# Performance work log

Measured on AMD Instinct MI355X. Metric: run time of the kernel, lower is better.

The kernel has to match this reference:

```python
import jax, jax.numpy as jnp
import numpy as np

B, S, D, H = 4, 2048, 1024, 16
DH = D // H  # head dim = 64
MASK_VALUE = -1000000.0


def setup_inputs() -> dict:
    key = jax.random.key(0)
    ks = jax.random.split(key, 8)
    return {
        "key": jax.random.normal(ks[0], (B, S, D), jnp.float32),
        "query": jax.random.normal(ks[1], (B, S, D), jnp.float32),
        "value": jax.random.normal(ks[2], (B, S, D), jnp.float32),
        "valid_lens": jax.random.randint(ks[3], (B,), 0, 2048, jnp.int32),
        # nn.Linear weights stored as [out_features, in_features]
        "Wk": jax.random.normal(ks[4], (D, D), jnp.float32) / np.sqrt(D),
        "Wq": jax.random.normal(ks[5], (D, D), jnp.float32) / np.sqrt(D),
        "Wv": jax.random.normal(ks[6], (D, D), jnp.float32) / np.sqrt(D),
        "Wo": jax.random.normal(ks[7], (D, D), jnp.float32) / np.sqrt(D),
    }


def _split_heads(x):
    # [B, S, D] -> [B, H, S, DH]
    return x.reshape(B, S, H, DH).transpose(0, 2, 1, 3)


def reference(key, query, value, valid_lens, Wk, Wq, Wv, Wo):
    # projections (Linear: x @ W^T, bias=False)
    q = _split_heads(query @ Wq.T)  # [B, H, S, DH]
    k = _split_heads(key @ Wk.T)
    v = _split_heads(value @ Wv.T)

    scale = 1.0 / jnp.sqrt(jnp.asarray(DH, q.dtype))
    scores = jnp.einsum("bhqd,bhkd->bhqk", q, k) * scale  # [B, H, S, S]

    # valid_lens masks the key axis per batch element (same for all heads/queries)
    key_mask = jnp.arange(S) < valid_lens[:, None]  # [B, S]
    scores = jnp.where(key_mask[:, None, None, :], scores, MASK_VALUE)

    attn = jax.nn.softmax(scores, axis=-1)
    out = jnp.einsum("bhqk,bhkd->bhqd", attn, v)  # [B, H, S, DH]
    out = out.transpose(0, 2, 1, 3).reshape(B, S, D)  # concat heads
    return out @ Wo.T
```

## Files before the change

### kernel.cpp

```cpp
#include <hip/hip_runtime.h>
#include <hip/hip_bf16.h>
#include <stdint.h>

typedef __bf16 bf16;
typedef __bf16 bf16x4 __attribute__((ext_vector_type(4)));
typedef __bf16 bf16x8 __attribute__((ext_vector_type(8)));
typedef float f32x4 __attribute__((ext_vector_type(4)));
typedef float f32x8 __attribute__((ext_vector_type(8)));

#define MFMA16 __builtin_amdgcn_mfma_f32_16x16x32_bf16

__device__ __forceinline__ void gload_lds16(void* lds, const void* g) {
  __builtin_amdgcn_global_load_lds(
      (const __attribute__((address_space(1))) unsigned int*)g,
      (__attribute__((address_space(3))) unsigned int*)lds, 16, 0, 0);
}

__global__ __launch_bounds__(256) void cvt1(const float* __restrict__ src,
                                            bf16* __restrict__ dst) {
  int i = (blockIdx.x * 256 + threadIdx.x) * 4;
  f32x4 v = *(const f32x4*)(src + i);
  bf16x4 o;
#pragma unroll
  for (int j = 0; j < 4; j++) o[j] = (bf16)v[j];
  *(bf16x4*)(dst + i) = o;
}

__global__ __launch_bounds__(256) void cvt4(const float* __restrict__ w0,
                                            const float* __restrict__ w1,
                                            const float* __restrict__ w2,
                                            const float* __restrict__ w3,
                                            bf16* __restrict__ dst) {
  const float* srcs[4] = {w0, w1, w2, w3};
  const float* src = srcs[blockIdx.y];
  int i = (blockIdx.x * 256 + threadIdx.x) * 4;
  f32x4 v = *(const f32x4*)(src + i);
  bf16x4 o;
#pragma unroll
  for (int j = 0; j < 4; j++) o[j] = (bf16)v[j];
  *(bf16x4*)(dst + (size_t)blockIdx.y * 1048576 + i) = o;
}

__device__ __forceinline__ void gemm_body(const bf16* __restrict__ A,
                                          const bf16* __restrict__ W,
                                          void* __restrict__ Craw, int mode,
                                          bf16* As, bf16* Bs) {
  constexpr int K = 1024;
  const int t = threadIdx.x;
  const int lane = t & 63;
  const int quad = lane >> 4;
  const int m16 = lane & 15;
  const int w = t >> 6;
  const int m0 = blockIdx.y * 128;
  const int n0 = blockIdx.x * 128;
  const int wm = (w >> 1) * 64;
  const int wn = (w & 1) * 64;

  f32x4 acc[4][4];
#pragma unroll
  for (int i = 0; i < 4; i++)
#pragma unroll
    for (int j = 0; j < 4; j++) acc[i][j] = (f32x4){0.f, 0.f, 0.f, 0.f};

  for (int kt = 0; kt < K / 32; kt++) {
    __syncthreads();
#pragma unroll
    for (int p = 0; p < 2; p++) {
      int idx = p * 256 + t;
      int row = idx >> 2;
      int ce = (idx & 3) * 8;
      gload_lds16(&As[idx * 8], A + (size_t)(m0 + row) * K + kt * 32 + ce);
      gload_lds16(&Bs[idx * 8], W + (size_t)(n0 + row) * K + kt * 32 + ce);
    }
    __syncthreads();

    bf16x8 af[4], bfr[4];
#pragma unroll
    for (int i = 0; i < 4; i++) {
      af[i] = *(const bf16x8*)&As[(wm + i * 16 + m16) * 32 + quad * 8];
      bfr[i] = *(const bf16x8*)&Bs[(wn + i * 16 + m16) * 32 + quad * 8];
    }
#pragma unroll
    for (int i = 0; i < 4; i++)
#pragma unroll
      for (int j = 0; j < 4; j++)
        acc[i][j] = MFMA16(af[i], bfr[j], acc[i][j], 0, 0, 0);
  }

#pragma unroll
  for (int i = 0; i < 4; i++) {
    int rbase = m0 + wm + i * 16 + quad * 4;
#pragma unroll
    for (int j = 0; j < 4; j++) {
      int col = n0 + wn + j * 16 + m16;
#pragma unroll
      for (int r = 0; r < 4; r++) {
        int row = rbase + r;
        if (mode == 0) {
          ((float*)Craw)[(size_t)row * 1024 + col] = acc[i][j][r];
        } else {
          int b = row >> 11, s = row & 2047;
          int h = col >> 6, d = col & 63;
          bf16 v = (bf16)acc[i][j][r];
          if (mode == 1)
            ((bf16*)Craw)[(((size_t)(b * 16 + h)) * 2048 + s) * 64 + d] = v;
          else
            ((bf16*)Craw)[(((size_t)(b * 16 + h)) * 64 + d) * 2048 + s] = v;
        }
      }
    }
  }
}

__global__ __launch_bounds__(256) void gemm_qkv(
    const bf16* __restrict__ xq, const bf16* __restrict__ xk,
    const bf16* __restrict__ xv, const bf16* __restrict__ wb,
    bf16* __restrict__ qp, bf16* __restrict__ kp, bf16* __restrict__ vt) {
  __shared__ bf16 As[128 * 32];
  __shared__ bf16 Bs[128 * 32];
  const int z = blockIdx.z;
  const bf16* A = (z == 0) ? xq : (z == 1) ? xk : xv;
  const bf16* W = wb + (size_t)z * 1048576;
  bf16* C = (z == 0) ? qp : (z == 1) ? kp : vt;
  gemm_body(A, W, C, (z == 2) ? 2 : 1, As, Bs);
}

__global__ __launch_bounds__(256) void gemm_one(const bf16* __restrict__ A,
                                                const bf16* __restrict__ W,
                                                void* __restrict__ Craw,
                                                int mode) {
  __shared__ bf16 As[128 * 32];
  __shared__ bf16 Bs[128 * 32];
  gemm_body(A, W, Craw, mode, As, Bs);
}

template <int AF32, int WF32>
__global__ __launch_bounds__(256) void gemm_bt(const void* __restrict__ Araw,
                                               const void* __restrict__ Wraw,
                                               void* __restrict__ Craw,
                                               int mode) {
  constexpr int K = 1024;
  __shared__ bf16 As[128 * 32];
  __shared__ bf16 Bs[128 * 32];
  const int t = threadIdx.x;
  const int lane = t & 63;
  const int quad = lane >> 4;
  const int m16 = lane & 15;
  const int w = t >> 6;
  const int m0 = blockIdx.y * 128;
  const int n0 = blockIdx.x * 128;
  const int wm = (w >> 1) * 64;
  const int wn = (w & 1) * 64;

  f32x4 acc[4][4];
#pragma unroll
  for (int i = 0; i < 4; i++)
#pragma unroll
    for (int j = 0; j < 4; j++) acc[i][j] = (f32x4){0.f, 0.f, 0.f, 0.f};

  for (int kt = 0; kt < K / 32; kt++) {
    bf16x8 aR[2], bR[2];
#pragma unroll
    for (int p = 0; p < 2; p++) {
      int idx = p * 256 + t;
      int row = idx >> 2;
      int ce = (idx & 3) * 8;
      size_t aoff = (size_t)(m0 + row) * K + kt * 32 + ce;
      size_t boff = (size_t)(n0 + row) * K + kt * 32 + ce;
      if constexpr (AF32) {
        f32x8 av = *(const f32x8*)((const float*)Araw + aoff);
#pragma unroll
        for (int j = 0; j < 8; j++) aR[p][j] = (bf16)av[j];
      } else {
        aR[p] = *(const bf16x8*)((const bf16*)Araw + aoff);
      }
      if constexpr (WF32) {
        f32x8 bv = *(const f32x8*)((const float*)Wraw + boff);
#pragma unroll
        for (int j = 0; j < 8; j++) bR[p][j] = (bf16)bv[j];
      } else {
        bR[p] = *(const bf16x8*)((const bf16*)Wraw + boff);
      }
    }
    __syncthreads();
#pragma unroll
    for (int p = 0; p < 2; p++) {
      int idx = p * 256 + t;
      *(bf16x8*)&As[idx * 8] = aR[p];
      *(bf16x8*)&Bs[idx * 8] = bR[p];
    }
    __syncthreads();

    bf16x8 af[4], bfr[4];
#pragma unroll
    for (int i = 0; i < 4; i++) {
      af[i] = *(const bf16x8*)&As[(wm + i * 16 + m16) * 32 + quad * 8];
      bfr[i] = *(const bf16x8*)&Bs[(wn + i * 16 + m16) * 32 + quad * 8];
    }
#pragma unroll
    for (int i = 0; i < 4; i++)
#pragma unroll
      for (int j = 0; j < 4; j++)
        acc[i][j] = MFMA16(af[i], bfr[j], acc[i][j], 0, 0, 0);
  }

#pragma unroll
  for (int i = 0; i < 4; i++) {
    int rbase = m0 + wm + i * 16 + quad * 4;
#pragma unroll
    for (int j = 0; j < 4; j++) {
      int col = n0 + wn + j * 16 + m16;
#pragma unroll
      for (int r = 0; r < 4; r++) {
        int row = rbase + r;
        if (mode == 0) {
          ((float*)Craw)[(size_t)row * 1024 + col] = acc[i][j][r];
        } else {
          int b = row >> 11, s = row & 2047;
          int h = col >> 6, d = col & 63;
          bf16 v = (bf16)acc[i][j][r];
          if (mode == 1)
            ((bf16*)Craw)[(((size_t)(b * 16 + h)) * 2048 + s) * 64 + d] = v;
          else
            ((bf16*)Craw)[(((size_t)(b * 16 + h)) * 64 + d) * 2048 + s] = v;
        }
      }
    }
  }
}

__global__ __launch_bounds__(256) void attn(const bf16* __restrict__ qp,
                                            const bf16* __restrict__ kp,
                                            const bf16* __restrict__ vt,
                                            const int* __restrict__ vlen,
                                            bf16* __restrict__ ctx) {
  __shared__ bf16 Ks[64 * 64];
  __shared__ bf16 Vs[64 * 64];
  __shared__ bf16 Ps[4 * 16 * 72];

  const int t = threadIdx.x;
  const int lane = t & 63;
  const int quad = lane >> 4;
  const int m16 = lane & 15;
  const int sw = m16 & 7;
  const int w = t >> 6;
  const int bh = blockIdx.y;
  const int qt = blockIdx.x;
  const int b = bh >> 4;
  const int h = bh & 15;
  const int vl = vlen[b];

  const float C1 = 0.18033688f;
  const float C2 = 46.166241f;
  const float mArg = (vl == 0) ? 0.0f : -12800.0f;

  const bf16* qbase = qp + ((size_t)(bh * 2048 + qt * 64 + w * 16 + m16)) * 64;
  bf16x8 qf[2];
  qf[0] = *(const bf16x8*)(qbase + quad * 8);
  qf[1] = *(const bf16x8*)(qbase + 32 + quad * 8);

  float rsum[4] = {0.f, 0.f, 0.f, 0.f};
  f32x4 o[4];
#pragma unroll
  for (int nt = 0; nt < 4; nt++) o[nt] = (f32x4){0.f, 0.f, 0.f, 0.f};

  const int ktEnd = (vl == 0) ? 32 : ((vl + 63) >> 6);

  for (int kt = 0; kt < ktEnd; kt++) {
    __syncthreads();
#pragma unroll
    for (int p = 0; p < 2; p++) {
      int idx = p * 256 + t;
      int row = idx >> 3;
      int gc = (idx & 7) ^ (row & 7);
      gload_lds16(&Ks[idx * 8],
                  &kp[((size_t)(bh * 2048 + kt * 64 + row)) * 64 + gc * 8]);
      gload_lds16(&Vs[idx * 8],
                  &vt[((size_t)(bh * 64 + row)) * 2048 + kt * 64 + gc * 8]);
    }
    __syncthreads();

    f32x4 s[4];
#pragma unroll
    for (int nt = 0; nt < 4; nt++) {
      f32x4 a = (f32x4){0.f, 0.f, 0.f, 0.f};
      int key = nt * 16 + m16;
#pragma unroll
      for (int ks = 0; ks < 2; ks++) {
        bf16x8 kf =
            *(const bf16x8*)&Ks[key * 64 + (((ks * 4 + quad) ^ sw) * 8)];
        a = MFMA16(qf[ks], kf, a, 0, 0, 0);
      }
      s[nt] = a;
    }

#pragma unroll
    for (int nt = 0; nt < 4; nt++) {
      bool masked = (kt * 64 + nt * 16 + m16) >= vl;
#pragma unroll
      for (int r = 0; r < 4; r++) {
        float arg = masked ? mArg : (s[nt][r] * C1 - C2);
        bf16 pb = (bf16)__builtin_amdgcn_exp2f(arg);
        rsum[r] += (float)pb;
        Ps[w * 1152 + (quad * 4 + r) * 72 + nt * 16 + m16] = pb;
      }
    }

#pragma unroll
    for (int ks = 0; ks < 2; ks++) {
      bf16x8 pf = *(const bf16x8*)&Ps[w * 1152 + m16 * 72 + ks * 32 + quad * 8];
#pragma unroll
      for (int nt = 0; nt < 4; nt++) {
        int dh = nt * 16 + m16;
        bf16x8 vf =
            *(const bf16x8*)&Vs[dh * 64 + (((ks * 4 + quad) ^ sw) * 8)];
        o[nt] = MFMA16(pf, vf, o[nt], 0, 0, 0);
      }
    }
  }

#pragma unroll
  for (int off = 1; off < 16; off <<= 1)
#pragma unroll
    for (int r = 0; r < 4; r++) rsum[r] += __shfl_xor(rsum[r], off);
#pragma unroll
  for (int r = 0; r < 4; r++) rsum[r] = 1.0f / rsum[r];

#pragma unroll
  for (int nt = 0; nt < 4; nt++) {
    int dh = nt * 16 + m16;
#pragma unroll
    for (int r = 0; r < 4; r++) {
      int srow = qt * 64 + w * 16 + quad * 4 + r;
      ctx[((size_t)(b * 2048 + srow)) * 1024 + h * 64 + dh] =
          (bf16)(o[nt][r] * rsum[r]);
    }
  }
}

extern "C" void kernel_launch(void* const* d_in, const int* in_sizes, int n_in,
                              void* d_out, int out_size, void* d_ws,
                              size_t ws_size, hipStream_t stream) {
  const float* key = (const float*)d_in[0];
  const float* query = (const float*)d_in[1];
  const float* value = (const float*)d_in[2];
  const int* vlen = (const int*)d_in[3];
  const float* Wk = (const float*)d_in[4];
  const float* Wq = (const float*)d_in[5];
  const float* Wv = (const float*)d_in[6];
  const float* Wo = (const float*)d_in[7];

  const size_t NE = (size_t)4 * 2048 * 1024;
  const size_t WE = 1048576;

  const size_t needA = (6 * NE + 4 * WE) * sizeof(bf16);
  const size_t needB = (5 * NE + 4 * WE) * sizeof(bf16);
  dim3 gg(8, 64), gb(256);

  if (ws_size >= needA) {
    bf16* qp = (bf16*)d_ws;
    bf16* kp = qp + NE;
    bf16* vt = kp + NE;
    bf16* xq = vt + NE;
    bf16* xk = xq + NE;
    bf16* xv = xk + NE;
    bf16* wb = xv + NE;
    bf16* ctx = xq;

    cvt4<<<dim3(1024, 4), gb, 0, stream>>>(Wq, Wk, Wv, Wo, wb);
    cvt1<<<8192, gb, 0, stream>>>(query, xq);
    cvt1<<<8192, gb, 0, stream>>>(key, xk);
    cvt1<<<8192, gb, 0, stream>>>(value, xv);
    gemm_qkv<<<dim3(8, 64, 3), gb, 0, stream>>>(xq, xk, xv, wb, qp, kp, vt);
    attn<<<dim3(32, 64), gb, 0, stream>>>(qp, kp, vt, vlen, ctx);
    gemm_one<<<gg, gb, 0, stream>>>(ctx, wb + 3 * WE, d_out, 0);
  } else if (ws_size >= needB) {
    bf16* qp = (bf16*)d_ws;
    bf16* kp = qp + NE;
    bf16* vt = kp + NE;
    bf16* ctx = vt + NE;
    bf16* xb = ctx + NE;
    bf16* wb = xb + NE;

    cvt4<<<dim3(1024, 4), gb, 0, stream>>>(Wq, Wk, Wv, Wo, wb);
    cvt1<<<8192, gb, 0, stream>>>(query, xb);
    gemm_one<<<gg, gb, 0, stream>>>(xb, wb + 0 * WE, qp, 1);
    cvt1<<<8192, gb, 0, stream>>>(key, xb);
    gemm_one<<<gg, gb, 0, stream>>>(xb, wb + 1 * WE, kp, 1);
    cvt1<<<8192, gb, 0, stream>>>(value, xb);
    gemm_one<<<gg, gb, 0, stream>>>(xb, wb + 2 * WE, vt, 2);
    attn<<<dim3(32, 64), gb, 0, stream>>>(qp, kp, vt, vlen, ctx);
    gemm_one<<<gg, gb, 0, stream>>>(ctx, wb + 3 * WE, d_out, 0);
  } else {
    bf16* qp = (bf16*)d_ws;
    bf16* kp = qp + NE;
    bf16* vt = kp + NE;
    bf16* ctx = vt + NE;
    gemm_bt<1, 1><<<gg, gb, 0, stream>>>(query, Wq, qp, 1);
    gemm_bt<1, 1><<<gg, gb, 0, stream>>>(key, Wk, kp, 1);
    gemm_bt<1, 1><<<gg, gb, 0, stream>>>(value, Wv, vt, 2);
    attn<<<dim3(32, 64), gb, 0, stream>>>(qp, kp, vt, vlen, ctx);
    gemm_bt<0, 1><<<gg, gb, 0, stream>>>(ctx, Wo, d_out, 0);
  }
}
```

Before: 355.6 us.

## Fuse input casts, remap GEMM tiles by XCD, skip masked K/V rows, double attention query tile

```diff
diff --git a/kernel.cpp b/kernel.cpp
--- a/kernel.cpp
+++ b/kernel.cpp
@@ -14,6 +14,22 @@
   __builtin_amdgcn_global_load_lds(
       (const __attribute__((address_space(1))) unsigned int*)g,
       (__attribute__((address_space(3))) unsigned int*)lds, 16, 0, 0);
+}
+
+__global__ __launch_bounds__(256) void cvt3(
+    const float* __restrict__ s0, const float* __restrict__ s1,
+    const float* __restrict__ s2, bf16* __restrict__ d0,
+    bf16* __restrict__ d1, bf16* __restrict__ d2) {
+  const float* srcs[3] = {s0, s1, s2};
+  bf16* dsts[3] = {d0, d1, d2};
+  const float* src = srcs[blockIdx.y];
+  bf16* dst = dsts[blockIdx.y];
+  int i = (blockIdx.x * 256 + threadIdx.x) * 4;
+  f32x4 v = *(const f32x4*)(src + i);
+  bf16x4 o;
+#pragma unroll
+  for (int j = 0; j < 4; j++) o[j] = (bf16)v[j];
+  *(bf16x4*)(dst + i) = o;
 }
 
 __global__ __launch_bounds__(256) void cvt1(const float* __restrict__ src,
@@ -41,18 +57,24 @@
   *(bf16x4*)(dst + (size_t)blockIdx.y * 1048576 + i) = o;
 }
 
+__device__ __forceinline__ void xcd_remap(int& m0, int& n0) {
+  int id = blockIdx.y * 8 + blockIdx.x;
+  int xcd = id & 7;
+  int j = id >> 3;
+  m0 = (xcd * 8 + (j >> 3)) * 128;
+  n0 = (j & 7) * 128;
+}
+
 __device__ __forceinline__ void gemm_body(const bf16* __restrict__ A,
                                           const bf16* __restrict__ W,
                                           void* __restrict__ Craw, int mode,
-                                          bf16* As, bf16* Bs) {
+                                          int m0, int n0, bf16* As, bf16* Bs) {
   constexpr int K = 1024;
   const int t = threadIdx.x;
   const int lane = t & 63;
   const int quad = lane >> 4;
   const int m16 = lane & 15;
   const int w = t >> 6;
-  const int m0 = blockIdx.y * 128;
-  const int n0 = blockIdx.x * 128;
   const int wm = (w >> 1) * 64;
   const int wn = (w & 1) * 64;
 
@@ -115,14 +137,23 @@
 __global__ __launch_bounds__(256) void gemm_qkv(
     const bf16* __restrict__ xq, const bf16* __restrict__ xk,
     const bf16* __restrict__ xv, const bf16* __restrict__ wb,
-    bf16* __restrict__ qp, bf16* __restrict__ kp, bf16* __restrict__ vt) {
+    const int* __restrict__ vlen, bf16* __restrict__ qp,
+    bf16* __restrict__ kp, bf16* __restrict__ vt) {
   __shared__ bf16 As[128 * 32];
   __shared__ bf16 Bs[128 * 32];
+  int m0, n0;
+  xcd_remap(m0, n0);
   const int z = blockIdx.z;
+  if (z >= 1) {
+    int b = m0 >> 11;
+    int s0 = m0 & 2047;
+    int vl = vlen[b];
+    if (vl != 0 && s0 >= vl) return;
+  }
   const bf16* A = (z == 0) ? xq : (z == 1) ? xk : xv;
   const bf16* W = wb + (size_t)z * 1048576;
   bf16* C = (z == 0) ? qp : (z == 1) ? kp : vt;
-  gemm_body(A, W, C, (z == 2) ? 2 : 1, As, Bs);
+  gemm_body(A, W, C, (z == 2) ? 2 : 1, m0, n0, As, Bs);
 }
 
 __global__ __launch_bounds__(256) void gemm_one(const bf16* __restrict__ A,
@@ -131,7 +162,9 @@
                                                 int mode) {
   __shared__ bf16 As[128 * 32];
   __shared__ bf16 Bs[128 * 32];
-  gemm_body(A, W, Craw, mode, As, Bs);
+  int m0, n0;
+  xcd_remap(m0, n0);
+  gemm_body(A, W, Craw, mode, m0, n0, As, Bs);
 }
 
 template <int AF32, int WF32>
@@ -236,7 +269,7 @@
                                             bf16* __restrict__ ctx) {
   __shared__ bf16 Ks[64 * 64];
   __shared__ bf16 Vs[64 * 64];
-  __shared__ bf16 Ps[4 * 16 * 72];
+  __shared__ bf16 Ps[4 * 32 * 72];
 
   const int t = threadIdx.x;
   const int lane = t & 63;
@@ -254,15 +287,21 @@
   const float C2 = 46.166241f;
   const float mArg = (vl == 0) ? 0.0f : -12800.0f;
 
-  const bf16* qbase = qp + ((size_t)(bh * 2048 + qt * 64 + w * 16 + m16)) * 64;
-  bf16x8 qf[2];
-  qf[0] = *(const bf16x8*)(qbase + quad * 8);
-  qf[1] = *(const bf16x8*)(qbase + 32 + quad * 8);
-
-  float rsum[4] = {0.f, 0.f, 0.f, 0.f};
-  f32x4 o[4];
-#pragma unroll
-  for (int nt = 0; nt < 4; nt++) o[nt] = (f32x4){0.f, 0.f, 0.f, 0.f};
+  bf16x8 qf[2][2];
+#pragma unroll
+  for (int a = 0; a < 2; a++) {
+    const bf16* qb =
+        qp + ((size_t)(bh * 2048 + qt * 128 + w * 32 + a * 16 + m16)) * 64;
+    qf[a][0] = *(const bf16x8*)(qb + quad * 8);
+    qf[a][1] = *(const bf16x8*)(qb + 32 + quad * 8);
+  }
+
+  float rsum[2][4] = {{0.f, 0.f, 0.f, 0.f}, {0.f, 0.f, 0.f, 0.f}};
+  f32x4 o[2][4];
+#pragma unroll
+  for (int a = 0; a < 2; a++)
+#pragma unroll
+    for (int nt = 0; nt < 4; nt++) o[a][nt] = (f32x4){0.f, 0.f, 0.f, 0.f};
 
   const int ktEnd = (vl == 0) ? 32 : ((vl + 63) >> 6);
 
@@ -280,41 +319,49 @@
     }
     __syncthreads();
 
-    f32x4 s[4];
+    f32x4 s[2][4];
+#pragma unroll
+    for (int a = 0; a < 2; a++)
+#pragma unroll
+      for (int nt = 0; nt < 4; nt++) s[a][nt] = (f32x4){0.f, 0.f, 0.f, 0.f};
 #pragma unroll
     for (int nt = 0; nt < 4; nt++) {
-      f32x4 a = (f32x4){0.f, 0.f, 0.f, 0.f};
       int key = nt * 16 + m16;
 #pragma unroll
       for (int ks = 0; ks < 2; ks++) {
         bf16x8 kf =
             *(const bf16x8*)&Ks[key * 64 + (((ks * 4 + quad) ^ sw) * 8)];
-        a = MFMA16(qf[ks], kf, a, 0, 0, 0);
-      }
-      s[nt] = a;
+        s[0][nt] = MFMA16(qf[0][ks], kf, s[0][nt], 0, 0, 0);
+        s[1][nt] = MFMA16(qf[1][ks], kf, s[1][nt], 0, 0, 0);
+      }
     }
 
 #pragma unroll
     for (int nt = 0; nt < 4; nt++) {
       bool masked = (kt * 64 + nt * 16 + m16) >= vl;
 #pragma unroll
-      for (int r = 0; r < 4; r++) {
-        float arg = masked ? mArg : (s[nt][r] * C1 - C2);
-        bf16 pb = (bf16)__builtin_amdgcn_exp2f(arg);
-        rsum[r] += (float)pb;
-        Ps[w * 1152 + (quad * 4 + r) * 72 + nt * 16 + m16] = pb;
-      }
+      for (int a = 0; a < 2; a++)
+#pragma unroll
+        for (int r = 0; r < 4; r++) {
+          float arg = masked ? mArg : (s[a][nt][r] * C1 - C2);
+          bf16 pb = (bf16)__builtin_amdgcn_exp2f(arg);
+          rsum[a][r] += (float)pb;
+          Ps[w * 2304 + (a * 16 + quad * 4 + r) * 72 + nt * 16 + m16] = pb;
+        }
     }
 
 #pragma unroll
     for (int ks = 0; ks < 2; ks++) {
-      bf16x8 pf = *(const bf16x8*)&Ps[w * 1152 + m16 * 72 + ks * 32 + quad * 8];
+      bf16x8 pf0 = *(const bf16x8*)&Ps[w * 2304 + m16 * 72 + ks * 32 + quad * 8];
+      bf16x8 pf1 =
+          *(const bf16x8*)&Ps[w * 2304 + (16 + m16) * 72 + ks * 32 + quad * 8];
 #pragma unroll
       for (int nt = 0; nt < 4; nt++) {
         int dh = nt * 16 + m16;
         bf16x8 vf =
             *(const bf16x8*)&Vs[dh * 64 + (((ks * 4 + quad) ^ sw) * 8)];
-        o[nt] = MFMA16(pf, vf, o[nt], 0, 0, 0);
+        o[0][nt] = MFMA16(pf0, vf, o[0][nt], 0, 0, 0);
+        o[1][nt] = MFMA16(pf1, vf, o[1][nt], 0, 0, 0);
       }
     }
   }
@@ -322,20 +369,26 @@
 #pragma unroll
   for (int off = 1; off < 16; off <<= 1)
 #pragma unroll
-    for (int r = 0; r < 4; r++) rsum[r] += __shfl_xor(rsum[r], off);
-#pragma unroll
-  for (int r = 0; r < 4; r++) rsum[r] = 1.0f / rsum[r];
-
-#pragma unroll
-  for (int nt = 0; nt < 4; nt++) {
-    int dh = nt * 16 + m16;
-#pragma unroll
-    for (int r = 0; r < 4; r++) {
-      int srow = qt * 64 + w * 16 + quad * 4 + r;
-      ctx[((size_t)(b * 2048 + srow)) * 1024 + h * 64 + dh] =
-          (bf16)(o[nt][r] * rsum[r]);
-    }
-  }
+    for (int a = 0; a < 2; a++)
+#pragma unroll
+      for (int r = 0; r < 4; r++) rsum[a][r] += __shfl_xor(rsum[a][r], off);
+#pragma unroll
+  for (int a = 0; a < 2; a++)
+#pragma unroll
+    for (int r = 0; r < 4; r++) rsum[a][r] = 1.0f / rsum[a][r];
+
+#pragma unroll
+  for (int a = 0; a < 2; a++)
+#pragma unroll
+    for (int nt = 0; nt < 4; nt++) {
+      int dh = nt * 16 + m16;
+#pragma unroll
+      for (int r = 0; r < 4; r++) {
+        int srow = qt * 128 + w * 32 + a * 16 + quad * 4 + r;
+        ctx[((size_t)(b * 2048 + srow)) * 1024 + h * 64 + dh] =
+            (bf16)(o[a][nt][r] * rsum[a][r]);
+      }
+    }
 }
 
 extern "C" void kernel_launch(void* const* d_in, const int* in_sizes, int n_in,
@@ -368,11 +421,10 @@
     bf16* ctx = xq;
 
     cvt4<<<dim3(1024, 4), gb, 0, stream>>>(Wq, Wk, Wv, Wo, wb);
-    cvt1<<<8192, gb, 0, stream>>>(query, xq);
-    cvt1<<<8192, gb, 0, stream>>>(key, xk);
-    cvt1<<<8192, gb, 0, stream>>>(value, xv);
-    gemm_qkv<<<dim3(8, 64, 3), gb, 0, stream>>>(xq, xk, xv, wb, qp, kp, vt);
-    attn<<<dim3(32, 64), gb, 0, stream>>>(qp, kp, vt, vlen, ctx);
+    cvt3<<<dim3(8192, 3), gb, 0, stream>>>(query, key, value, xq, xk, xv);
+    gemm_qkv<<<dim3(8, 64, 3), gb, 0, stream>>>(xq, xk, xv, wb, vlen, qp, kp,
+                                                vt);
+    attn<<<dim3(16, 64), gb, 0, stream>>>(qp, kp, vt, vlen, ctx);
     gemm_one<<<gg, gb, 0, stream>>>(ctx, wb + 3 * WE, d_out, 0);
   } else if (ws_size >= needB) {
     bf16* qp = (bf16*)d_ws;
@@ -389,7 +441,7 @@
     gemm_one<<<gg, gb, 0, stream>>>(xb, wb + 1 * WE, kp, 1);
     cvt1<<<8192, gb, 0, stream>>>(value, xb);
     gemm_one<<<gg, gb, 0, stream>>>(xb, wb + 2 * WE, vt, 2);
-    attn<<<dim3(32, 64), gb, 0, stream>>>(qp, kp, vt, vlen, ctx);
+    attn<<<dim3(16, 64), gb, 0, stream>>>(qp, kp, vt, vlen, ctx);
     gemm_one<<<gg, gb, 0, stream>>>(ctx, wb + 3 * WE, d_out, 0);
   } else {
     bf16* qp = (bf16*)d_ws;
@@ -399,7 +451,7 @@
     gemm_bt<1, 1><<<gg, gb, 0, stream>>>(query, Wq, qp, 1);
     gemm_bt<1, 1><<<gg, gb, 0, stream>>>(key, Wk, kp, 1);
     gemm_bt<1, 1><<<gg, gb, 0, stream>>>(value, Wv, vt, 2);
-    attn<<<dim3(32, 64), gb, 0, stream>>>(qp, kp, vt, vlen, ctx);
+    attn<<<dim3(16, 64), gb, 0, stream>>>(qp, kp, vt, vlen, ctx);
     gemm_bt<0, 1><<<gg, gb, 0, stream>>>(ctx, Wo, d_out, 0);
   }
 }
```

Measured after the change: 335.4 us. -5.7%, faster.
